# Performance work log

Measured on AMD Instinct MI355X. Metric: run time of the kernel, lower is better.

The kernel has to match this reference:

```python
import jax, jax.numpy as jnp
import numpy as np

N_NODES = 50000
N_EDGES = 1600000
IN_DIM, HIDDEN, OUT_DIM = 128, 128, 64


def setup_inputs() -> dict:
    key = jax.random.key(0)
    ks = jax.random.split(key, 8)
    x = jax.random.normal(ks[0], (N_NODES, IN_DIM), dtype=jnp.float32)
    edge_index = jax.random.randint(ks[1], (2, N_EDGES), 0, N_NODES, dtype=jnp.int64)
    # SAGEConv params: lin_l applied to aggregated neighbors (with bias),
    # lin_r applied to root/self features (no bias) -- PyG defaults.
    def lin_init(k, fan_in, fan_out):
        bound = 1.0 / np.sqrt(fan_in)
        return jax.random.uniform(k, (fan_in, fan_out), jnp.float32, -bound, bound)
    W1_l = lin_init(ks[2], IN_DIM, HIDDEN)
    W1_r = lin_init(ks[3], IN_DIM, HIDDEN)
    b1 = jnp.zeros((HIDDEN,), jnp.float32)
    W2_l = lin_init(ks[4], HIDDEN, OUT_DIM)
    W2_r = lin_init(ks[5], HIDDEN, OUT_DIM)
    b2 = jnp.zeros((OUT_DIM,), jnp.float32)
    return {"x": x, "edge_index": edge_index, "W1_l": W1_l, "W1_r": W1_r,
            "b1": b1, "W2_l": W2_l, "W2_r": W2_r, "b2": b2}


def _sage_conv(h, src, dst, n_nodes, W_l, W_r, b):
    # gather messages from source nodes, mean-aggregate at destinations
    msg = h[src]                                              # [E, D]
    agg_sum = jax.ops.segment_sum(msg, dst, num_segments=n_nodes)
    deg = jax.ops.segment_sum(jnp.ones((src.shape[0],), h.dtype), dst,
                              num_segments=n_nodes)
    agg_mean = agg_sum / jnp.maximum(deg, 1.0)[:, None]       # [N, D]
    return agg_mean @ W_l + h @ W_r + b


def reference(x, edge_index, W1_l, W1_r, b1, W2_l, W2_r, b2):
    n = x.shape[0]
    src, dst = edge_index[0], edge_index[1]
    h = jax.nn.relu(_sage_conv(x, src, dst, n, W1_l, W1_r, b1))
    return _sage_conv(h, src, dst, n, W2_l, W2_r, b2)
```

## Files before the change

kernel.cpp:

```cpp
#include <hip/hip_runtime.h>

#define NN 50000
#define NE 1600000
#define BSTRIDE 96
#define BNODES 100
#define C_BKT 500
#define P1_BLKS 512
#define P1_CHUNK 3125
#define CAP 32
#define XCVT_BLKS 1563
#define WCVT_BLKS 48
#define PP_PREP (XCVT_BLKS + WCVT_BLKS)
#define RGRP 3128

typedef __bf16 bf16x8 __attribute__((ext_vector_type(8)));
typedef float  f32x4  __attribute__((ext_vector_type(4)));
typedef float  f32x2  __attribute__((ext_vector_type(2)));

__device__ __forceinline__ float bfLo(uint u) { union { uint i; float f; } v; v.i = u << 16; return v.f; }
__device__ __forceinline__ float bfHi(uint u) { union { uint i; float f; } v; v.i = u & 0xffff0000u; return v.f; }
__device__ __forceinline__ ushort f2bf(float f) {
    union { float f; uint i; } v; v.f = f;
    uint r = v.i + 0x7fffu + ((v.i >> 16) & 1u);
    return (ushort)(r >> 16);
}
__device__ __forceinline__ uint pack2(float a, float b) {
    return (uint)f2bf(a) | ((uint)f2bf(b) << 16);
}
__device__ __forceinline__ bf16x8 load8(const ushort* p) {
    union { uint4 u; bf16x8 b; } v; v.u = *(const uint4*)p; return v.b;
}

#define ACC8(u) { a0 += bfLo(u.x); a1 += bfHi(u.x); a2 += bfLo(u.y); a3 += bfHi(u.y); \
                  a4 += bfLo(u.z); a5 += bfHi(u.z); a6 += bfLo(u.w); a7 += bfHi(u.w); }

#define CVA(u, o) { f32x2 p0 = __builtin_amdgcn_cvt_pk_f32_fp8((int)(u), 0); \
                    f32x2 p1 = __builtin_amdgcn_cvt_pk_f32_fp8((int)(u), 1); \
                    a[(o)+0] += p0.x; a[(o)+1] += p0.y; a[(o)+2] += p1.x; a[(o)+3] += p1.y; }
#define ACCF8(v) { CVA((v).x, 0); CVA((v).y, 4); CVA((v).z, 8); CVA((v).w, 12); }

__device__ __forceinline__ int pkOff(int n, int k) {
    return (((n >> 4) * 4 + (k >> 5)) * 512) + (((k >> 3) & 3) * 128) + ((n & 15) * 8) + (k & 7);
}

__global__ __launch_bounds__(1024) void k_pp(
    const float4* __restrict__ x, ushort* __restrict__ xbp, uint* __restrict__ xf8,
    const float* __restrict__ W1l, const float* __restrict__ W1r,
    const float* __restrict__ W2l, const float* __restrict__ W2r,
    ushort* __restrict__ T1l, ushort* __restrict__ T1r,
    ushort* __restrict__ T2l, ushort* __restrict__ T2r,
    const int* __restrict__ src, const int* __restrict__ dst,
    uint* __restrict__ cells, ushort* __restrict__ cnt) {
    __shared__ uint hist[C_BKT];
    const int b = blockIdx.x;
    const int tid = threadIdx.x;
    if (b < XCVT_BLKS) {
        int i = b * 1024 + tid;
        if (i < NN * 128 / 4) {
            float4 v = x[i];
            int r = i >> 5, k0 = (i & 31) * 4;
            ushort4 o; o.x = f2bf(v.x); o.y = f2bf(v.y); o.z = f2bf(v.z); o.w = f2bf(v.w);
            *(ushort4*)(xbp + pkOff(r, k0)) = o;
            uint rr = (uint)__builtin_amdgcn_cvt_pk_fp8_f32(v.x, v.y, 0, 0);
            rr = (uint)__builtin_amdgcn_cvt_pk_fp8_f32(v.z, v.w, (int)rr, 1);
            xf8[i] = rr;
        }
    } else if (b < PP_PREP) {
        int i = (b - XCVT_BLKS) * 1024 + tid;
        if (i < 16384) {
            int k = i >> 7, n = i & 127; T1l[pkOff(n, k)] = f2bf(W1l[i]);
        } else if (i < 32768) {
            int j = i - 16384; int k = j >> 7, n = j & 127; T1r[pkOff(n, k)] = f2bf(W1r[j]);
        } else if (i < 40960) {
            int j = i - 32768; int k = j >> 6, n = j & 63;  T2l[pkOff(n, k)] = f2bf(W2l[j]);
        } else {
            int j = i - 40960; int k = j >> 6, n = j & 63;  T2r[pkOff(n, k)] = f2bf(W2r[j]);
        }
    } else {
        const int b2 = b - PP_PREP;
        for (int i = tid; i < C_BKT; i += 1024) hist[i] = 0;
        __syncthreads();
        const int beg = b2 * P1_CHUNK;
        uint* myCells = cells + (size_t)b2 * C_BKT * CAP;
        for (int i = beg + tid; i < beg + P1_CHUNK; i += 1024) {
            int d = dst[i];
            int s = src[i];
            int c = d / BNODES;
            uint p = atomicAdd(&hist[c], 1);
            if (p < CAP) myCells[c * CAP + p] = ((uint)(d - c * BNODES) << 16) | (uint)s;
        }
        __syncthreads();
        for (int i = tid; i < C_BKT; i += 1024)
            cnt[(size_t)b2 * C_BKT + i] = (ushort)min(hist[i], (uint)CAP);
    }
}

__global__ __launch_bounds__(1024) void k_pagg(
    const uint* __restrict__ cells, const ushort* __restrict__ cnt,
    const uchar* __restrict__ xf8, ushort* __restrict__ col,
    int* __restrict__ deg, ushort* __restrict__ aggp) {
    __shared__ uint hist[BNODES];
    __shared__ __align__(16) ushort colS[BNODES * BSTRIDE];
    const int c = blockIdx.x;
    const int tid = threadIdx.x;
    if (tid < BNODES) hist[tid] = 0;
    __syncthreads();
    {
        const int b = tid >> 1, sub = tid & 1;
        const uint* cell = cells + ((size_t)b * C_BKT + c) * CAP;
        const int n = cnt[(size_t)b * C_BKT + c];
        for (int j = sub; j < n; j += 2) {
            uint e = cell[j];
            int dl = e >> 16;
            uint p = atomicAdd(&hist[dl], 1);
            if (p < BSTRIDE) colS[dl * BSTRIDE + p] = (ushort)(e & 0xFFFF);
        }
    }
    __syncthreads();
    const int nodeBase = c * BNODES;
    if (tid < BNODES) deg[nodeBase + tid] = (int)hist[tid];
    {
        uint4* cg = (uint4*)(col + (size_t)nodeBase * BSTRIDE);
        const uint4* cs = (const uint4*)colS;
        for (int i = tid; i < BNODES * BSTRIDE / 8; i += 1024) cg[i] = cs[i];
    }
    const int wave = tid >> 6, lane = tid & 63;
    const int q = lane >> 3;
    const int cc = lane & 7;
    for (int ln = wave; ln < BNODES; ln += 16) {
        int d = (int)hist[ln];
        int dd = min(d, BSTRIDE);
        const ushort* cb = &colS[ln * BSTRIDE];
        float a[16];
        #pragma unroll
        for (int i = 0; i < 16; i++) a[i] = 0.f;
        for (int j0 = 0; j0 < dd; j0 += 64) {
            int idx = (j0 + lane < dd) ? (int)cb[j0 + lane] : 0;
            int cnt2 = min(64, dd - j0);
            int t = 0;
            for (; t + 32 <= cnt2; t += 32) {
                int s0 = __shfl(idx, t + q);
                int s1 = __shfl(idx, t + 8 + q);
                int s2 = __shfl(idx, t + 16 + q);
                int s3 = __shfl(idx, t + 24 + q);
                uint4 u0 = *(const uint4*)(xf8 + (size_t)s0 * 128 + cc * 16);
                uint4 u1 = *(const uint4*)(xf8 + (size_t)s1 * 128 + cc * 16);
                uint4 u2 = *(const uint4*)(xf8 + (size_t)s2 * 128 + cc * 16);
                uint4 u3 = *(const uint4*)(xf8 + (size_t)s3 * 128 + cc * 16);
                ACCF8(u0); ACCF8(u1); ACCF8(u2); ACCF8(u3);
            }
            for (; t + 16 <= cnt2; t += 16) {
                int s0 = __shfl(idx, t + q);
                int s1 = __shfl(idx, t + 8 + q);
                uint4 u0 = *(const uint4*)(xf8 + (size_t)s0 * 128 + cc * 16);
                uint4 u1 = *(const uint4*)(xf8 + (size_t)s1 * 128 + cc * 16);
                ACCF8(u0); ACCF8(u1);
            }
            for (; t < cnt2; t += 8) {
                int s = __shfl(idx, t + q);
                if (t + q < cnt2) {
                    uint4 u = *(const uint4*)(xf8 + (size_t)s * 128 + cc * 16);
                    ACCF8(u);
                }
            }
        }
        #pragma unroll
        for (int m = 8; m < 64; m <<= 1) {
            #pragma unroll
            for (int i = 0; i < 16; i++) a[i] += __shfl_xor(a[i], m);
        }
        if (q == 0) {
            int node = nodeBase + ln;
            float inv = 1.f / fmaxf((float)d, 1.f);
            int base = ((node >> 4) * 4 + (cc >> 1)) * 512 + ((cc & 1) * 2) * 128 + (node & 15) * 8;
            uint4 o;
            o.x = pack2(a[0] * inv, a[1] * inv);
            o.y = pack2(a[2] * inv, a[3] * inv);
            o.z = pack2(a[4] * inv, a[5] * inv);
            o.w = pack2(a[6] * inv, a[7] * inv);
            *(uint4*)(aggp + base) = o;
            o.x = pack2(a[8] * inv, a[9] * inv);
            o.y = pack2(a[10] * inv, a[11] * inv);
            o.z = pack2(a[12] * inv, a[13] * inv);
            o.w = pack2(a[14] * inv, a[15] * inv);
            *(uint4*)(aggp + base + 128) = o;
        }
    }
}

#define PAD1 136
__global__ __launch_bounds__(256) void k_gemm12(
    const ushort* __restrict__ aggp, const ushort* __restrict__ xbp,
    const ushort* __restrict__ T1l, const ushort* __restrict__ T1r,
    const ushort* __restrict__ T2l, const ushort* __restrict__ T2r,
    const float* __restrict__ b1, const float* __restrict__ b2,
    ushort* __restrict__ hW, float* __restrict__ outp) {
    __shared__ ushort hS[2][16 * PAD1];
    const int lane = threadIdx.x & 63;
    const int wave = threadIdx.x >> 6;
    const int s = wave >> 1;
    const int ch = wave & 1;
    const int quad = lane >> 4, r16 = lane & 15;
    const int row0 = blockIdx.x * 32 + s * 16;
    const int g = blockIdx.x * 2 + s;
    ushort* myS = &hS[s][0];

    f32x4 acc[4];
    #pragma unroll
    for (int nt = 0; nt < 4; nt++) acc[nt] = (f32x4){0.f, 0.f, 0.f, 0.f};
    #pragma unroll
    for (int kt = 0; kt < 4; kt++) {
        bf16x8 aAgg = load8(aggp + (size_t)(g * 4 + kt) * 512 + lane * 8);
        bf16x8 aXb  = load8(xbp  + (size_t)(g * 4 + kt) * 512 + lane * 8);
        #pragma unroll
        for (int nt = 0; nt < 4; nt++) {
            const int tile = ((ch * 4 + nt) * 4 + kt) * 512 + lane * 8;
            acc[nt] = __builtin_amdgcn_mfma_f32_16x16x32_bf16(aAgg, load8(T1l + tile), acc[nt], 0, 0, 0);
            acc[nt] = __builtin_amdgcn_mfma_f32_16x16x32_bf16(aXb,  load8(T1r + tile), acc[nt], 0, 0, 0);
        }
    }
    #pragma unroll
    for (int nt = 0; nt < 4; nt++) {
        int cc = ch * 64 + nt * 16 + r16;
        float bv = b1[cc];
        #pragma unroll
        for (int i = 0; i < 4; i++)
            myS[(quad * 4 + i) * PAD1 + cc] = f2bf(fmaxf(acc[nt][i] + bv, 0.f));
    }
    __syncthreads();

    f32x4 acc2[2], acc3[2];
    #pragma unroll
    for (int nt = 0; nt < 2; nt++) {
        acc2[nt] = (f32x4){0.f, 0.f, 0.f, 0.f};
        acc3[nt] = (f32x4){0.f, 0.f, 0.f, 0.f};
    }
    #pragma unroll
    for (int kt = 0; kt < 4; kt++) {
        bf16x8 ah = load8(&myS[r16 * PAD1 + kt * 32 + quad * 8]);
        #pragma unroll
        for (int nt = 0; nt < 2; nt++) {
            const int tile = ((ch * 2 + nt) * 4 + kt) * 512 + lane * 8;
            acc2[nt] = __builtin_amdgcn_mfma_f32_16x16x32_bf16(ah, load8(T2l + tile), acc2[nt], 0, 0, 0);
            acc3[nt] = __builtin_amdgcn_mfma_f32_16x16x32_bf16(ah, load8(T2r + tile), acc3[nt], 0, 0, 0);
        }
    }
    #pragma unroll
    for (int nt = 0; nt < 2; nt++) {
        int cc = ch * 32 + nt * 16 + r16;
        float bv = b2[cc];
        #pragma unroll
        for (int i = 0; i < 4; i++) {
            int rr = row0 + quad * 4 + i;
            if (rr < NN) {
                hW[(size_t)rr * 64 + cc] = f2bf(acc2[nt][i]);
                outp[(size_t)rr * 64 + cc] = acc3[nt][i] + bv;
            }
        }
    }
}

__global__ void k_agg64f(const ushort* __restrict__ hW, const ushort* __restrict__ col,
                         const int* __restrict__ deg, const float* __restrict__ outp,
                         float* __restrict__ out) {
    int node = (blockIdx.x * blockDim.x + threadIdx.x) >> 6;
    int lane = threadIdx.x & 63;
    int q = lane >> 3;
    int c = lane & 7;
    int d = deg[node];
    int dd = min(d, BSTRIDE);
    const ushort* cb = col + (size_t)node * BSTRIDE;
    float a0=0.f,a1=0.f,a2=0.f,a3=0.f,a4=0.f,a5=0.f,a6=0.f,a7=0.f;
    for (int j0 = 0; j0 < dd; j0 += 64) {
        int idx = (j0 + lane < dd) ? (int)cb[j0 + lane] : 0;
        int cnt = min(64, dd - j0);
        int t = 0;
        for (; t + 16 <= cnt; t += 16) {
            int s0 = __shfl(idx, t + q);
            int s1 = __shfl(idx, t + 8 + q);
            uint4 u0 = *(const uint4*)(hW + (size_t)s0 * 64 + c * 8);
            uint4 u1 = *(const uint4*)(hW + (size_t)s1 * 64 + c * 8);
            ACC8(u0); ACC8(u1);
        }
        for (; t < cnt; t += 8) {
            int s = __shfl(idx, t + q);
            if (t + q < cnt) {
                uint4 u = *(const uint4*)(hW + (size_t)s * 64 + c * 8);
                ACC8(u);
            }
        }
    }
    #pragma unroll
    for (int m = 8; m < 64; m <<= 1) {
        a0 += __shfl_xor(a0, m); a1 += __shfl_xor(a1, m);
        a2 += __shfl_xor(a2, m); a3 += __shfl_xor(a3, m);
        a4 += __shfl_xor(a4, m); a5 += __shfl_xor(a5, m);
        a6 += __shfl_xor(a6, m); a7 += __shfl_xor(a7, m);
    }
    if (q == 0) {
        float inv = 1.f / fmaxf((float)d, 1.f);
        float4 p0 = *(const float4*)(outp + (size_t)node * 64 + c * 8);
        float4 p1 = *(const float4*)(outp + (size_t)node * 64 + c * 8 + 4);
        float4 o;
        o.x = a0 * inv + p0.x; o.y = a1 * inv + p0.y;
        o.z = a2 * inv + p0.z; o.w = a3 * inv + p0.w;
        *(float4*)(out + (size_t)node * 64 + c * 8) = o;
        o.x = a4 * inv + p1.x; o.y = a5 * inv + p1.y;
        o.z = a6 * inv + p1.z; o.w = a7 * inv + p1.w;
        *(float4*)(out + (size_t)node * 64 + c * 8 + 4) = o;
    }
}

extern "C" void kernel_launch(void* const* d_in, const int* in_sizes, int n_in,
                              void* d_out, int out_size, void* d_ws, size_t ws_size,
                              hipStream_t stream) {
    const float* x   = (const float*)d_in[0];
    const int*   ei  = (const int*)d_in[1];
    const float* W1l = (const float*)d_in[2];
    const float* W1r = (const float*)d_in[3];
    const float* b1  = (const float*)d_in[4];
    const float* W2l = (const float*)d_in[5];
    const float* W2r = (const float*)d_in[6];
    const float* b2  = (const float*)d_in[7];
    float* out = (float*)d_out;

    const int* src = ei;
    const int* dst = ei + NE;

    char* w = (char*)d_ws;
    ushort* col   = (ushort*)w;                  w += (size_t)NN * BSTRIDE * 2;
    int* deg      = (int*)w;                     w += (size_t)50048 * 4;
    ushort* cnt   = (ushort*)w;                  w += (size_t)P1_BLKS * C_BKT * 2;
    ushort* xbp   = (ushort*)w;                  w += (size_t)RGRP * 2048 * 2;
    ushort* T1l   = (ushort*)w;                  w += 128 * 128 * 2;
    ushort* T1r   = (ushort*)w;                  w += 128 * 128 * 2;
    ushort* T2l   = (ushort*)w;                  w += 64 * 128 * 2;
    ushort* T2r   = (ushort*)w;                  w += 64 * 128 * 2;
    ushort* aggp  = (ushort*)w;                  w += (size_t)RGRP * 2048 * 2;
    ushort* hW    = (ushort*)w;                  w += (size_t)NN * 64 * 2;
    float* outp   = (float*)w;                   w += (size_t)NN * 64 * 4;
    uchar* xf8    = (uchar*)w;                   w += (size_t)NN * 128;
    uint* cells   = (uint*)w;                    w += (size_t)P1_BLKS * C_BKT * CAP * 4;

    k_pp<<<PP_PREP + P1_BLKS, 1024, 0, stream>>>(
        (const float4*)x, xbp, (uint*)xf8, W1l, W1r, W2l, W2r,
        T1l, T1r, T2l, T2r, src, dst, cells, cnt);

    k_pagg<<<C_BKT, 1024, 0, stream>>>(cells, cnt, xf8, col, deg, aggp);

    k_gemm12<<<(NN + 31) / 32, 256, 0, stream>>>(aggp, xbp, T1l, T1r, T2l, T2r, b1, b2, hW, outp);

    k_agg64f<<<NN / 4, 256, 0, stream>>>(hW, col, deg, outp, out);
}
```

Baseline: 206.5 us.

## Replace fixed-capacity bucket cells with per-block counting-sort offsets

Phase-1 binning now does a two-pass counting sort per block (histogram, prefix scan, then scatter into a compact per-block array with packed start/count offsets) instead of fixed-capacity CAP=32 slots that could drop edges. Buckets shrink to 50 nodes (1000 buckets) with fewer, larger edge chunks (128 blocks), and the aggregation kernel uses 512-thread blocks with an interleaved bucket order. The aim is to remove the padded sparse cell storage and improve occupancy and load balance. In exchange the dst array is read twice and there are extra scan barriers.

Result: slower. 213.0 us (+3.1%).

```diff
diff --git a/kernel.cpp b/kernel.cpp
--- a/kernel.cpp
+++ b/kernel.cpp
@@ -3,11 +3,10 @@
 #define NN 50000
 #define NE 1600000
 #define BSTRIDE 96
-#define BNODES 100
-#define C_BKT 500
-#define P1_BLKS 512
-#define P1_CHUNK 3125
-#define CAP 32
+#define BNODES 50
+#define C_BKT 1000
+#define P1_BLKS 128
+#define P1_CHUNK 12500
 #define XCVT_BLKS 1563
 #define WCVT_BLKS 48
 #define PP_PREP (XCVT_BLKS + WCVT_BLKS)
@@ -50,8 +49,9 @@
     ushort* __restrict__ T1l, ushort* __restrict__ T1r,
     ushort* __restrict__ T2l, ushort* __restrict__ T2r,
     const int* __restrict__ src, const int* __restrict__ dst,
-    uint* __restrict__ cells, ushort* __restrict__ cnt) {
-    __shared__ uint hist[C_BKT];
+    uint* __restrict__ cells, uint* __restrict__ offc) {
+    __shared__ uint hist[C_BKT + 1];
+    __shared__ uint part[128];
     const int b = blockIdx.x;
     const int tid = threadIdx.x;
     if (b < XCVT_BLKS) {
@@ -81,35 +81,69 @@
         for (int i = tid; i < C_BKT; i += 1024) hist[i] = 0;
         __syncthreads();
         const int beg = b2 * P1_CHUNK;
-        uint* myCells = cells + (size_t)b2 * C_BKT * CAP;
+        for (int i = beg + tid; i < beg + P1_CHUNK; i += 1024) {
+            int c = dst[i] / BNODES;
+            atomicAdd(&hist[c], 1);
+        }
+        __syncthreads();
+        if (tid < 125) {
+            uint s = 0;
+            #pragma unroll
+            for (int k = 0; k < 8; k++) {
+                uint t = hist[tid * 8 + k];
+                hist[tid * 8 + k] = s;
+                s += t;
+            }
+            part[tid] = s;
+        }
+        __syncthreads();
+        if (tid == 0) {
+            uint run = 0;
+            for (int t = 0; t < 125; t++) { uint tmp = part[t]; part[t] = run; run += tmp; }
+        }
+        __syncthreads();
+        if (tid < 125) {
+            uint bs = part[tid];
+            if (bs) {
+                #pragma unroll
+                for (int k = 0; k < 8; k++) hist[tid * 8 + k] += bs;
+            }
+        }
+        __syncthreads();
+        for (int c = tid; c < C_BKT; c += 1024) {
+            uint st = hist[c];
+            uint en = (c == C_BKT - 1) ? (uint)P1_CHUNK : hist[c + 1];
+            offc[(size_t)b2 * C_BKT + c] = st | ((en - st) << 16);
+        }
+        __syncthreads();
+        uint* myCells = cells + (size_t)b2 * P1_CHUNK;
         for (int i = beg + tid; i < beg + P1_CHUNK; i += 1024) {
             int d = dst[i];
             int s = src[i];
             int c = d / BNODES;
             uint p = atomicAdd(&hist[c], 1);
-            if (p < CAP) myCells[c * CAP + p] = ((uint)(d - c * BNODES) << 16) | (uint)s;
-        }
-        __syncthreads();
-        for (int i = tid; i < C_BKT; i += 1024)
-            cnt[(size_t)b2 * C_BKT + i] = (ushort)min(hist[i], (uint)CAP);
-    }
-}
-
-__global__ __launch_bounds__(1024) void k_pagg(
-    const uint* __restrict__ cells, const ushort* __restrict__ cnt,
+            myCells[p] = ((uint)(d - c * BNODES) << 16) | (uint)s;
+        }
+    }
+}
+
+__global__ __launch_bounds__(512) void k_pagg(
+    const uint* __restrict__ cells, const uint* __restrict__ offc,
     const uchar* __restrict__ xf8, ushort* __restrict__ col,
     int* __restrict__ deg, ushort* __restrict__ aggp) {
     __shared__ uint hist[BNODES];
     __shared__ __align__(16) ushort colS[BNODES * BSTRIDE];
-    const int c = blockIdx.x;
+    const int bid = blockIdx.x;
+    const int c = (bid & 7) * 125 + (bid >> 3);
     const int tid = threadIdx.x;
     if (tid < BNODES) hist[tid] = 0;
     __syncthreads();
     {
-        const int b = tid >> 1, sub = tid & 1;
-        const uint* cell = cells + ((size_t)b * C_BKT + c) * CAP;
-        const int n = cnt[(size_t)b * C_BKT + c];
-        for (int j = sub; j < n; j += 2) {
+        const int b = tid >> 2, sub = tid & 3;
+        uint v = offc[(size_t)b * C_BKT + c];
+        int st = (int)(v & 0xFFFF), n = (int)(v >> 16);
+        const uint* cell = cells + (size_t)b * P1_CHUNK + st;
+        for (int j = sub; j < n; j += 4) {
             uint e = cell[j];
             int dl = e >> 16;
             uint p = atomicAdd(&hist[dl], 1);
@@ -122,12 +156,12 @@
     {
         uint4* cg = (uint4*)(col + (size_t)nodeBase * BSTRIDE);
         const uint4* cs = (const uint4*)colS;
-        for (int i = tid; i < BNODES * BSTRIDE / 8; i += 1024) cg[i] = cs[i];
+        for (int i = tid; i < BNODES * BSTRIDE / 8; i += 512) cg[i] = cs[i];
     }
     const int wave = tid >> 6, lane = tid & 63;
     const int q = lane >> 3;
     const int cc = lane & 7;
-    for (int ln = wave; ln < BNODES; ln += 16) {
+    for (int ln = wave; ln < BNODES; ln += 8) {
         int d = (int)hist[ln];
         int dd = min(d, BSTRIDE);
         const ushort* cb = &colS[ln * BSTRIDE];
@@ -330,7 +364,7 @@
     char* w = (char*)d_ws;
     ushort* col   = (ushort*)w;                  w += (size_t)NN * BSTRIDE * 2;
     int* deg      = (int*)w;                     w += (size_t)50048 * 4;
-    ushort* cnt   = (ushort*)w;                  w += (size_t)P1_BLKS * C_BKT * 2;
+    uint* offc    = (uint*)w;                    w += (size_t)P1_BLKS * C_BKT * 4;
     ushort* xbp   = (ushort*)w;                  w += (size_t)RGRP * 2048 * 2;
     ushort* T1l   = (ushort*)w;                  w += 128 * 128 * 2;
     ushort* T1r   = (ushort*)w;                  w += 128 * 128 * 2;
@@ -340,13 +374,13 @@
     ushort* hW    = (ushort*)w;                  w += (size_t)NN * 64 * 2;
     float* outp   = (float*)w;                   w += (size_t)NN * 64 * 4;
     uchar* xf8    = (uchar*)w;                   w += (size_t)NN * 128;
-    uint* cells   = (uint*)w;                    w += (size_t)P1_BLKS * C_BKT * CAP * 4;
+    uint* cells   = (uint*)w;                    w += (size_t)NE * 4;
 
     k_pp<<<PP_PREP + P1_BLKS, 1024, 0, stream>>>(
         (const float4*)x, xbp, (uint*)xf8, W1l, W1r, W2l, W2r,
-        T1l, T1r, T2l, T2r, src, dst, cells, cnt);
-
-    k_pagg<<<C_BKT, 1024, 0, stream>>>(cells, cnt, xf8, col, deg, aggp);
+        T1l, T1r, T2l, T2r, src, dst, cells, offc);
+
+    k_pagg<<<C_BKT, 512, 0, stream>>>(cells, offc, xf8, col, deg, aggp);
 
     k_gemm12<<<(NN + 31) / 32, 256, 0, stream>>>(aggp, xbp, T1l, T1r, T2l, T2r, b1, b2, hW, outp);
 
```
